# Performance work log

Hardware: AMD Instinct MI355X
Metric: run time of the kernel (lower is better)

Reference implementation:

```python
import jax, jax.numpy as jnp
import numpy as np

NUM_HEADS = 8
KERNEL = 3


def _arsinh_norm(x, w, b):
    # ArsinhNorm with scale=1.0: weight * asinh(x) + bias
    return w * jnp.arcsinh(x) + b


def _nbr_idx(L, k):
    # NATTEN neighborhood: window start clamped so the k-window stays in-bounds
    start = jnp.clip(jnp.arange(L) - k // 2, 0, L - k)
    return start[:, None] + jnp.arange(k)  # [L, k]


def _na2d(x, qkv_w, qkv_b, proj_w, proj_b, num_heads=NUM_HEADS, k=KERNEL):
    B, H, W, C = x.shape
    hd = C // num_heads
    qkv = x @ qkv_w + qkv_b                      # [B,H,W,3C]
    q, kk, v = jnp.split(qkv, 3, axis=-1)
    q = q.reshape(B, H, W, num_heads, hd) * (hd ** -0.5)
    kk = kk.reshape(B, H, W, num_heads, hd)
    v = v.reshape(B, H, W, num_heads, hd)
    ri = _nbr_idx(H, k)[:, None, :, None]        # [H,1,k,1]
    ci = _nbr_idx(W, k)[None, :, None, :]        # [1,W,1,k]
    nb_k = kk[:, ri, ci].reshape(B, H, W, k * k, num_heads, hd)  # gather 3x3 neighborhood
    nb_v = v[:, ri, ci].reshape(B, H, W, k * k, num_heads, hd)
    scores = jnp.einsum('bijnd,bijmnd->bijnm', q, nb_k)          # [B,H,W,nh,k*k]
    attn = jax.nn.softmax(scores, axis=-1)
    out = jnp.einsum('bijnm,bijmnd->bijnd', attn, nb_v).reshape(B, H, W, C)
    return out @ proj_w + proj_b


def setup_inputs() -> dict:
    key = jax.random.key(0)
    ks = jax.random.split(key, 8)
    B, H, W, C = 16, 64, 64, 256
    s = 0.02
    return {
        'h': jax.random.normal(ks[0], (B, H, W, C), dtype=jnp.float32),
        'qkv_w': jax.random.normal(ks[1], (C, 3 * C), dtype=jnp.float32) * s,
        'qkv_b': jnp.zeros((3 * C,), jnp.float32),
        'proj_w': jax.random.normal(ks[2], (C, C), dtype=jnp.float32) * s,
        'proj_b': jnp.zeros((C,), jnp.float32),
        'n1_w': jnp.ones((C,), jnp.float32),
        'n1_b': jnp.zeros((C,), jnp.float32),
        'n2_w': jnp.ones((C,), jnp.float32),
        'n2_b': jnp.zeros((C,), jnp.float32),
        'mlp_w1': jax.random.normal(ks[3], (C, 2 * C), dtype=jnp.float32) * s,
        'mlp_b1': jnp.zeros((2 * C,), jnp.float32),
        'mlp_w2': jax.random.normal(ks[4], (2 * C, C), dtype=jnp.float32) * s,
        'mlp_b2': jnp.zeros((C,), jnp.float32),
    }


def reference(h, qkv_w, qkv_b, proj_w, proj_b, n1_w, n1_b, n2_w, n2_b,
              mlp_w1, mlp_b1, mlp_w2, mlp_b2):
    h1 = _arsinh_norm(h, n1_w, n1_b)
    h = h + _na2d(h1, qkv_w, qkv_b, proj_w, proj_b)
    h2 = _arsinh_norm(h, n2_w, n2_b)
    ff = jax.nn.gelu(h2 @ mlp_w1 + mlp_b1, approximate=False) @ mlp_w2 + mlp_b2
    return h + ff
```

## Files before the change

### kernel.cpp

```cpp
#include <hip/hip_runtime.h>
#include <math.h>

typedef unsigned short u16;
typedef unsigned int u32;
typedef __attribute__((ext_vector_type(8))) short short8;
typedef __attribute__((ext_vector_type(4))) float f32x4;

__device__ __forceinline__ float b2f(u16 u) {
    return __uint_as_float(((u32)u) << 16);
}
__device__ __forceinline__ u16 f2b(float f) {
    u32 x = __float_as_uint(f);
    return (u16)((x + 0x7fffu + ((x >> 16) & 1u)) >> 16);
}
__device__ __forceinline__ float ldext(const void* p, size_t i, int isbf) {
    return isbf ? b2f(((const u16*)p)[i]) : ((const float*)p)[i];
}
__device__ __forceinline__ void stext(void* p, size_t i, int isbf, float v) {
    if (isbf) ((u16*)p)[i] = f2b(v);
    else ((float*)p)[i] = v;
}
__device__ __forceinline__ float fast_asinh(float x) {
    float ax = fabsf(x);
    float s = sqrtf(fmaf(ax, ax, 1.f));
    float l = __logf(ax + s);
    return copysignf(l, x);
}
__device__ __forceinline__ float fast_gelu(float x) {
    float x2 = x * x;
    float inner = fmaf(0.044715f * x2, x, x);
    float t = __expf(1.5957691216057308f * inner);
    return x * t * __builtin_amdgcn_rcpf(t + 1.f);
}
__device__ __forceinline__ void gl2lds16(const u16* g, u16* l) {
    __builtin_amdgcn_global_load_lds(
        (const __attribute__((address_space(1))) u32*)(const void*)g,
        (__attribute__((address_space(3))) u32*)(void*)l, 16, 0, 0);
}
__device__ __forceinline__ void unpack8(uint4 w, float* f) {
    const u32* pw = (const u32*)&w;
#pragma unroll
    for (int k = 0; k < 4; ++k) {
        f[2 * k]     = __uint_as_float(pw[k] << 16);
        f[2 * k + 1] = __uint_as_float(pw[k] & 0xffff0000u);
    }
}

__global__ void detect_k(const void* __restrict__ h, int* __restrict__ flag) {
    __shared__ int cnt;
    if (threadIdx.x == 0) cnt = 0;
    __syncthreads();
    const u16* p = (const u16*)h;
    int local = 0;
    for (int i = threadIdx.x; i < 4096; i += 256) {
        int e = (p[i] >> 7) & 0xFF;
        if (e != 0 && (e < 110 || e > 133)) local++;
    }
    atomicAdd(&cnt, local);
    __syncthreads();
    if (threadIdx.x == 0) *flag = (cnt < 256) ? 1 : 0;
}

__global__ void transpose_k(const void* __restrict__ src, u16* __restrict__ dst,
                            int R, int C, const int* __restrict__ flag) {
    int isbf = *flag;
    int idx = blockIdx.x * 256 + threadIdx.x;
    if (idx >= R * C) return;
    int r = idx / C, c = idx - r * C;
    dst[c * R + r] = f2b(ldext(src, idx, isbf));
}

__global__ void norm_k(const void* __restrict__ xb, size_t xoff,
                       const void* __restrict__ w, const void* __restrict__ b,
                       u16* __restrict__ y, const int* __restrict__ flag, int force_bf) {
    int isbf = *flag;
    int xisbf = force_bf ? 1 : isbf;
    size_t base = ((size_t)blockIdx.x * 256 + threadIdx.x) * 4;
    int c0 = (int)(base & 255);
    float v[4];
    if (xisbf) {
        uint2 raw = *reinterpret_cast<const uint2*>((const u16*)xb + xoff + base);
        const u16* px = reinterpret_cast<const u16*>(&raw);
#pragma unroll
        for (int j = 0; j < 4; ++j) v[j] = b2f(px[j]);
    } else {
        float4 r = *reinterpret_cast<const float4*>((const float*)xb + xoff + base);
        v[0] = r.x; v[1] = r.y; v[2] = r.z; v[3] = r.w;
    }
    u16 o[4];
#pragma unroll
    for (int j = 0; j < 4; ++j)
        o[j] = f2b(ldext(w, c0 + j, isbf) * fast_asinh(v[j]) + ldext(b, c0 + j, isbf));
    *reinterpret_cast<uint2*>(y + base) = *reinterpret_cast<uint2*>(o);
}

template <int EPI>
__global__ __launch_bounds__(256) void gemm_bt(
    const u16* __restrict__ A, const u16* __restrict__ BT, const void* __restrict__ bias,
    const void* __restrict__ resb, size_t resoff, void* __restrict__ outb, size_t outoff,
    int N, int K, const int* __restrict__ flag,
    const void* __restrict__ n2w, const void* __restrict__ n2b, u16* __restrict__ out2) {
    __shared__ __align__(16) u16 lA[2][128 * 32];
    __shared__ __align__(16) u16 lB[2][128 * 32];
    const int isbf = *flag;
    const int tid = threadIdx.x;
    const int lane = tid & 63;
    const int wave = tid >> 6;
    const int waveM = wave >> 1, waveN = wave & 1;

    const int gx = gridDim.x;
    int nblk = gx * gridDim.y;
    int bflat = blockIdx.y * gx + blockIdx.x;
    int L = bflat;
    if ((nblk & 7) == 0) {
        int per = nblk >> 3;
        L = (bflat & 7) * per + (bflat >> 3);
    }
    const int m0 = (L / gx) * 128;
    const int n0 = (L % gx) * 128;

    f32x4 acc[4][4];
#pragma unroll
    for (int mi = 0; mi < 4; ++mi)
#pragma unroll
        for (int ni = 0; ni < 4; ++ni)
#pragma unroll
            for (int r = 0; r < 4; ++r) acc[mi][ni][r] = 0.f;

    const int lrow = lane & 15;
    const int ko = (lane >> 4) * 8;
    const int s0 = wave * 2, s1 = wave * 2 + 1;
    const int e0a = (s0 * 64 + lane) * 8, e1a = (s1 * 64 + lane) * 8;
    const int row0 = e0a >> 5, col0 = e0a & 31;
    const int row1 = e1a >> 5, col1 = e1a & 31;

    const int NT = K >> 5;
    gl2lds16(&A[(size_t)(m0 + row0) * K + col0], &lA[0][s0 * 512]);
    gl2lds16(&BT[(size_t)(n0 + row0) * K + col0], &lB[0][s0 * 512]);
    gl2lds16(&A[(size_t)(m0 + row1) * K + col1], &lA[0][s1 * 512]);
    gl2lds16(&BT[(size_t)(n0 + row1) * K + col1], &lB[0][s1 * 512]);
    __syncthreads();

    int cur = 0;
    for (int t = 0; t < NT; ++t) {
        if (t + 1 < NT) {
            int k0 = (t + 1) << 5;
            gl2lds16(&A[(size_t)(m0 + row0) * K + k0 + col0], &lA[cur ^ 1][s0 * 512]);
            gl2lds16(&BT[(size_t)(n0 + row0) * K + k0 + col0], &lB[cur ^ 1][s0 * 512]);
            gl2lds16(&A[(size_t)(m0 + row1) * K + k0 + col1], &lA[cur ^ 1][s1 * 512]);
            gl2lds16(&BT[(size_t)(n0 + row1) * K + k0 + col1], &lB[cur ^ 1][s1 * 512]);
        }
        short8 af[4], bfr[4];
#pragma unroll
        for (int mi = 0; mi < 4; ++mi)
            af[mi] = *reinterpret_cast<const short8*>(&lA[cur][(waveM * 64 + mi * 16 + lrow) * 32 + ko]);
#pragma unroll
        for (int ni = 0; ni < 4; ++ni)
            bfr[ni] = *reinterpret_cast<const short8*>(&lB[cur][(waveN * 64 + ni * 16 + lrow) * 32 + ko]);
#pragma unroll
        for (int mi = 0; mi < 4; ++mi)
#pragma unroll
            for (int ni = 0; ni < 4; ++ni)
                acc[mi][ni] = __builtin_amdgcn_mfma_f32_16x16x32_bf16(af[mi], bfr[ni], acc[mi][ni], 0, 0, 0);
        __syncthreads();
        cur ^= 1;
    }

    const int rquad = (lane >> 4) * 4;
    const int ccol = lane & 15;
#pragma unroll
    for (int mi = 0; mi < 4; ++mi)
#pragma unroll
        for (int ni = 0; ni < 4; ++ni) {
            int colg = n0 + waveN * 64 + ni * 16 + ccol;
            float bb = ldext(bias, colg, isbf);
#pragma unroll
            for (int r = 0; r < 4; ++r) {
                int rowg = m0 + waveM * 64 + mi * 16 + rquad + r;
                size_t idx = (size_t)rowg * N + colg;
                float v = acc[mi][ni][r] + bb;
                if (EPI == 0) {
                    ((u16*)outb)[outoff + idx] = f2b(v);
                } else if (EPI == 1) {
                    ((u16*)outb)[outoff + idx] = f2b(fast_gelu(v));
                } else if (EPI == 2) {
                    v += ldext(resb, resoff + idx, isbf);
                    stext(outb, outoff + idx, isbf, v);
                } else if (EPI == 3) {
                    v += ldext(resb, resoff + idx, isbf);
                    ((u16*)outb)[outoff + idx] = f2b(v);
                } else if (EPI == 4) {
                    v += b2f(((const u16*)resb)[resoff + idx]);
                    stext(outb, outoff + idx, isbf, v);
                } else {
                    v += ldext(resb, resoff + idx, isbf);
                    ((u16*)outb)[outoff + idx] = f2b(v);
                    float y = ldext(n2w, colg, isbf) * fast_asinh(v) + ldext(n2b, colg, isbf);
                    out2[idx] = f2b(y);
                }
            }
        }
}

__global__ __launch_bounds__(256) void attn_k(const u16* __restrict__ qkv, u16* __restrict__ out) {
    const int t = blockIdx.x * 256 + threadIdx.x;
    const int head = t & 7;
    const int p = t >> 3;
    const int b = p >> 12;
    const int ij = p & 4095;
    const int i = ij >> 6, j = ij & 63;
    int r0 = i - 1; r0 = r0 < 0 ? 0 : (r0 > 61 ? 61 : r0);
    int c0 = j - 1; c0 = c0 < 0 ? 0 : (c0 > 61 ? 61 : c0);

    const u16* qp = qkv + (size_t)p * 768 + head * 32;
    float q[32];
#pragma unroll
    for (int ch = 0; ch < 4; ++ch)
        unpack8(*reinterpret_cast<const uint4*>(qp + ch * 8), q + ch * 8);

    const float qscale = 0.17677669529663687f;
    int nbp[9];
    float sc[9];
#pragma unroll
    for (int dr = 0; dr < 3; ++dr)
#pragma unroll
        for (int dc = 0; dc < 3; ++dc) {
            int nb = dr * 3 + dc;
            int np_ = b * 4096 + (r0 + dr) * 64 + (c0 + dc);
            nbp[nb] = np_;
            const u16* kp = qkv + (size_t)np_ * 768 + 256 + head * 32;
            float dot = 0.f;
#pragma unroll
            for (int ch = 0; ch < 4; ++ch) {
                float kf[8];
                unpack8(*reinterpret_cast<const uint4*>(kp + ch * 8), kf);
#pragma unroll
                for (int e = 0; e < 8; ++e) dot += q[ch * 8 + e] * kf[e];
            }
            sc[nb] = dot * qscale;
        }

    float mx = sc[0];
#pragma unroll
    for (int nb = 1; nb < 9; ++nb) mx = fmaxf(mx, sc[nb]);
    float s = 0.f;
#pragma unroll
    for (int nb = 0; nb < 9; ++nb) { sc[nb] = __expf(sc[nb] - mx); s += sc[nb]; }
    float inv = 1.f / s;

    float acc[32];
#pragma unroll
    for (int e = 0; e < 32; ++e) acc[e] = 0.f;
#pragma unroll
    for (int nb = 0; nb < 9; ++nb) {
        const u16* vp = qkv + (size_t)nbp[nb] * 768 + 512 + head * 32;
        float wgt = sc[nb] * inv;
#pragma unroll
        for (int ch = 0; ch < 4; ++ch) {
            float vf[8];
            unpack8(*reinterpret_cast<const uint4*>(vp + ch * 8), vf);
#pragma unroll
            for (int e = 0; e < 8; ++e) acc[ch * 8 + e] += wgt * vf[e];
        }
    }

    u16 ob[32];
#pragma unroll
    for (int e = 0; e < 32; ++e) ob[e] = f2b(acc[e]);
    uint4* ov = reinterpret_cast<uint4*>(ob);
    uint4* og = reinterpret_cast<uint4*>(out + (size_t)p * 256 + head * 32);
#pragma unroll
    for (int ch = 0; ch < 4; ++ch) og[ch] = ov[ch];
}

extern "C" void kernel_launch(void* const* d_in, const int* in_sizes, int n_in,
                              void* d_out, int out_size, void* d_ws, size_t ws_size,
                              hipStream_t stream) {
    const void* h      = d_in[0];
    const void* qkv_w  = d_in[1];
    const void* qkv_b  = d_in[2];
    const void* proj_w = d_in[3];
    const void* proj_b = d_in[4];
    const void* n1_w   = d_in[5];
    const void* n1_b   = d_in[6];
    const void* n2_w   = d_in[7];
    const void* n2_b   = d_in[8];
    const void* w1     = d_in[9];
    const void* b1     = d_in[10];
    const void* w2     = d_in[11];
    const void* b2     = d_in[12];

    char* ws = (char*)d_ws;
    u16* WqkvT  = (u16*)(ws + 0);
    u16* WprojT = (u16*)(ws + 393216);
    u16* W1T    = (u16*)(ws + 524288);
    u16* W2T    = (u16*)(ws + 786432);
    int* Flag   = (int*)(ws + 1048576);
    char* bufs  = ws + 1049600;

    size_t avail = ws_size > 1049600 ? ws_size - 1049600 : 0;
    int CHUNK = 4096;
    if (avail >= (size_t)65536 * 2048) CHUNK = 65536;
    else if (avail >= (size_t)16384 * 2048) CHUNK = 16384;
    else if (avail >= (size_t)8192 * 2048) CHUNK = 8192;

    u16* H1 = (u16*)bufs;
    u16* S  = (u16*)(bufs + (size_t)CHUNK * 512);

    detect_k<<<1, 256, 0, stream>>>(h, Flag);
    transpose_k<<<768, 256, 0, stream>>>(qkv_w, WqkvT, 256, 768, Flag);
    transpose_k<<<256, 256, 0, stream>>>(proj_w, WprojT, 256, 256, Flag);
    transpose_k<<<512, 256, 0, stream>>>(w1, W1T, 256, 512, Flag);
    transpose_k<<<512, 256, 0, stream>>>(w2, W2T, 512, 256, Flag);

    if (CHUNK == 65536) {
        u16* HNS = S;
        u16* T   = S + (size_t)65536 * 256;
        u16* N2  = (u16*)d_out;
        norm_k<<<16384, 256, 0, stream>>>(h, 0, n1_w, n1_b, H1, Flag, 0);
        { dim3 g(6, 512); gemm_bt<0><<<g, 256, 0, stream>>>(H1, WqkvT, qkv_b, nullptr, 0, S, 0,
                                                            768, 256, Flag, nullptr, nullptr, nullptr); }
        attn_k<<<2048, 256, 0, stream>>>(S, H1);
        { dim3 g(2, 512); gemm_bt<5><<<g, 256, 0, stream>>>(H1, WprojT, proj_b, h, 0, HNS, 0,
                                                            256, 256, Flag, n2_w, n2_b, N2); }
        { dim3 g(4, 512); gemm_bt<1><<<g, 256, 0, stream>>>(N2, W1T, b1, nullptr, 0, T, 0,
                                                            512, 256, Flag, nullptr, nullptr, nullptr); }
        { dim3 g(2, 512); gemm_bt<4><<<g, 256, 0, stream>>>(T, W2T, b2, HNS, 0, d_out, 0,
                                                            256, 512, Flag, nullptr, nullptr, nullptr); }
    } else {
        const int NCH = 65536 / CHUNK;
        for (int c = 0; c < NCH; ++c) {
            size_t off = (size_t)c * CHUNK * 256;
            norm_k<<<CHUNK / 4, 256, 0, stream>>>(h, off, n1_w, n1_b, H1, Flag, 0);
            { dim3 g(6, CHUNK / 128);
              gemm_bt<0><<<g, 256, 0, stream>>>(H1, WqkvT, qkv_b, nullptr, 0, S, 0,
                                                768, 256, Flag, nullptr, nullptr, nullptr); }
            attn_k<<<CHUNK / 32, 256, 0, stream>>>(S, H1);
            { dim3 g(2, CHUNK / 128);
              gemm_bt<2><<<g, 256, 0, stream>>>(H1, WprojT, proj_b, h, off, d_out, off,
                                                256, 256, Flag, nullptr, nullptr, nullptr); }
        }
        for (int c = 0; c < NCH; ++c) {
            size_t off = (size_t)c * CHUNK * 256;
            norm_k<<<CHUNK / 4, 256, 0, stream>>>(d_out, off, n2_w, n2_b, H1, Flag, 0);
            { dim3 g(4, CHUNK / 128);
              gemm_bt<1><<<g, 256, 0, stream>>>(H1, W1T, b1, nullptr, 0, S, 0,
                                                512, 256, Flag, nullptr, nullptr, nullptr); }
            { dim3 g(2, CHUNK / 128);
              gemm_bt<2><<<g, 256, 0, stream>>>(S, W2T, b2, d_out, off, d_out, off,
                                                256, 512, Flag, nullptr, nullptr, nullptr); }
        }
    }
}
```

Baseline: 448.5 us.

## Triple-buffer GEMM LDS tiles with vmcnt waits and a single barrier per step

Changes the GEMM main loop from double to triple buffering in LDS. It prefetches two K-tiles ahead and uses explicit s_waitcnt vmcnt plus one barrier per iteration instead of a trailing __syncthreads. K becomes a template parameter so the loop can be fully unrolled with constant addressing. This is meant to hide global-to-LDS latency and cut synchronization overhead, but it raises LDS use from 32KB to 48KB per block, which may reduce occupancy. The vmcnt counting has to match the number of outstanding loads exactly.

```diff
diff --git a/kernel.cpp b/kernel.cpp
--- a/kernel.cpp
+++ b/kernel.cpp
@@ -94,14 +94,14 @@
     *reinterpret_cast<uint2*>(y + base) = *reinterpret_cast<uint2*>(o);
 }
 
-template <int EPI>
+template <int EPI, int K>
 __global__ __launch_bounds__(256) void gemm_bt(
     const u16* __restrict__ A, const u16* __restrict__ BT, const void* __restrict__ bias,
     const void* __restrict__ resb, size_t resoff, void* __restrict__ outb, size_t outoff,
-    int N, int K, const int* __restrict__ flag,
+    int N, const int* __restrict__ flag,
     const void* __restrict__ n2w, const void* __restrict__ n2b, u16* __restrict__ out2) {
-    __shared__ __align__(16) u16 lA[2][128 * 32];
-    __shared__ __align__(16) u16 lB[2][128 * 32];
+    __shared__ __align__(16) u16 lA[3][128 * 32];
+    __shared__ __align__(16) u16 lB[3][128 * 32];
     const int isbf = *flag;
     const int tid = threadIdx.x;
     const int lane = tid & 63;
@@ -134,36 +134,43 @@
     const int row0 = e0a >> 5, col0 = e0a & 31;
     const int row1 = e1a >> 5, col1 = e1a & 31;
 
-    const int NT = K >> 5;
-    gl2lds16(&A[(size_t)(m0 + row0) * K + col0], &lA[0][s0 * 512]);
-    gl2lds16(&BT[(size_t)(n0 + row0) * K + col0], &lB[0][s0 * 512]);
-    gl2lds16(&A[(size_t)(m0 + row1) * K + col1], &lA[0][s1 * 512]);
-    gl2lds16(&BT[(size_t)(n0 + row1) * K + col1], &lB[0][s1 * 512]);
-    __syncthreads();
-
-    int cur = 0;
+    constexpr int NT = K >> 5;
+    auto STAGE = [&](int kt, int bsel) {
+        int k0 = kt << 5;
+        gl2lds16(&A[(size_t)(m0 + row0) * K + k0 + col0], &lA[bsel][s0 * 512]);
+        gl2lds16(&BT[(size_t)(n0 + row0) * K + k0 + col0], &lB[bsel][s0 * 512]);
+        gl2lds16(&A[(size_t)(m0 + row1) * K + k0 + col1], &lA[bsel][s1 * 512]);
+        gl2lds16(&BT[(size_t)(n0 + row1) * K + k0 + col1], &lB[bsel][s1 * 512]);
+    };
+
+    STAGE(0, 0);
+    STAGE(1, 1);
+
+#pragma unroll
     for (int t = 0; t < NT; ++t) {
         if (t + 1 < NT) {
-            int k0 = (t + 1) << 5;
-            gl2lds16(&A[(size_t)(m0 + row0) * K + k0 + col0], &lA[cur ^ 1][s0 * 512]);
-            gl2lds16(&BT[(size_t)(n0 + row0) * K + k0 + col0], &lB[cur ^ 1][s0 * 512]);
-            gl2lds16(&A[(size_t)(m0 + row1) * K + k0 + col1], &lA[cur ^ 1][s1 * 512]);
-            gl2lds16(&BT[(size_t)(n0 + row1) * K + k0 + col1], &lB[cur ^ 1][s1 * 512]);
-        }
+            asm volatile("s_waitcnt vmcnt(4)" ::: "memory");
+        } else {
+            asm volatile("s_waitcnt vmcnt(0)" ::: "memory");
+        }
+        __builtin_amdgcn_s_barrier();
+        __builtin_amdgcn_sched_barrier(0);
+        if (t + 2 < NT) STAGE(t + 2, (t + 2) % 3);
+
+        const u16* la = lA[t % 3];
+        const u16* lb = lB[t % 3];
         short8 af[4], bfr[4];
 #pragma unroll
         for (int mi = 0; mi < 4; ++mi)
-            af[mi] = *reinterpret_cast<const short8*>(&lA[cur][(waveM * 64 + mi * 16 + lrow) * 32 + ko]);
+            af[mi] = *reinterpret_cast<const short8*>(&la[(waveM * 64 + mi * 16 + lrow) * 32 + ko]);
 #pragma unroll
         for (int ni = 0; ni < 4; ++ni)
-            bfr[ni] = *reinterpret_cast<const short8*>(&lB[cur][(waveN * 64 + ni * 16 + lrow) * 32 + ko]);
+            bfr[ni] = *reinterpret_cast<const short8*>(&lb[(waveN * 64 + ni * 16 + lrow) * 32 + ko]);
 #pragma unroll
         for (int mi = 0; mi < 4; ++mi)
 #pragma unroll
             for (int ni = 0; ni < 4; ++ni)
                 acc[mi][ni] = __builtin_amdgcn_mfma_f32_16x16x32_bf16(af[mi], bfr[ni], acc[mi][ni], 0, 0, 0);
-        __syncthreads();
-        cur ^= 1;
     }
 
     const int rquad = (lane >> 4) * 4;
@@ -318,37 +325,37 @@
         u16* T   = S + (size_t)65536 * 256;
         u16* N2  = (u16*)d_out;
         norm_k<<<16384, 256, 0, stream>>>(h, 0, n1_w, n1_b, H1, Flag, 0);
-        { dim3 g(6, 512); gemm_bt<0><<<g, 256, 0, stream>>>(H1, WqkvT, qkv_b, nullptr, 0, S, 0,
-                                                            768, 256, Flag, nullptr, nullptr, nullptr); }
+        { dim3 g(6, 512); gemm_bt<0, 256><<<g, 256, 0, stream>>>(H1, WqkvT, qkv_b, nullptr, 0, S, 0,
+                                                                 768, Flag, nullptr, nullptr, nullptr); }
         attn_k<<<2048, 256, 0, stream>>>(S, H1);
-        { dim3 g(2, 512); gemm_bt<5><<<g, 256, 0, stream>>>(H1, WprojT, proj_b, h, 0, HNS, 0,
-                                                            256, 256, Flag, n2_w, n2_b, N2); }
-        { dim3 g(4, 512); gemm_bt<1><<<g, 256, 0, stream>>>(N2, W1T, b1, nullptr, 0, T, 0,
-                                                            512, 256, Flag, nullptr, nullptr, nullptr); }
-        { dim3 g(2, 512); gemm_bt<4><<<g, 256, 0, stream>>>(T, W2T, b2, HNS, 0, d_out, 0,
-                                                            256, 512, Flag, nullptr, nullptr, nullptr); }
+        { dim3 g(2, 512); gemm_bt<5, 256><<<g, 256, 0, stream>>>(H1, WprojT, proj_b, h, 0, HNS, 0,
+                                                                 256, Flag, n2_w, n2_b, N2); }
+        { dim3 g(4, 512); gemm_bt<1, 256><<<g, 256, 0, stream>>>(N2, W1T, b1, nullptr, 0, T, 0,
+                                                                 512, Flag, nullptr, nullptr, nullptr); }
+        { dim3 g(2, 512); gemm_bt<4, 512><<<g, 256, 0, stream>>>(T, W2T, b2, HNS, 0, d_out, 0,
+                                                                 256, Flag, nullptr, nullptr, nullptr); }
     } else {
         const int NCH = 65536 / CHUNK;
         for (int c = 0; c < NCH; ++c) {
             size_t off = (size_t)c * CHUNK * 256;
             norm_k<<<CHUNK / 4, 256, 0, stream>>>(h, off, n1_w, n1_b, H1, Flag, 0);
             { dim3 g(6, CHUNK / 128);
-              gemm_bt<0><<<g, 256, 0, stream>>>(H1, WqkvT, qkv_b, nullptr, 0, S, 0,
-                                                768, 256, Flag, nullptr, nullptr, nullptr); }
+              gemm_bt<0, 256><<<g, 256, 0, stream>>>(H1, WqkvT, qkv_b, nullptr, 0, S, 0,
+                                                     768, Flag, nullptr, nullptr, nullptr); }
             attn_k<<<CHUNK / 32, 256, 0, stream>>>(S, H1);
             { dim3 g(2, CHUNK / 128);
-              gemm_bt<2><<<g, 256, 0, stream>>>(H1, WprojT, proj_b, h, off, d_out, off,
-                                                256, 256, Flag, nullptr, nullptr, nullptr); }
+              gemm_bt<2, 256><<<g, 256, 0, stream>>>(H1, WprojT, proj_b, h, off, d_out, off,
+                                                     256, Flag, nullptr, nullptr, nullptr); }
         }
         for (int c = 0; c < NCH; ++c) {
             size_t off = (size_t)c * CHUNK * 256;
             norm_k<<<CHUNK / 4, 256, 0, stream>>>(d_out, off, n2_w, n2_b, H1, Flag, 0);
             { dim3 g(4, CHUNK / 128);
-              gemm_bt<1><<<g, 256, 0, stream>>>(H1, W1T, b1, nullptr, 0, S, 0,
-                                                512, 256, Flag, nullptr, nullptr, nullptr); }
+              gemm_bt<1, 256><<<g, 256, 0, stream>>>(H1, W1T, b1, nullptr, 0, S, 0,
+                                                     512, Flag, nullptr, nullptr, nullptr); }
             { dim3 g(2, CHUNK / 128);
-              gemm_bt<2><<<g, 256, 0, stream>>>(S, W2T, b2, d_out, off, d_out, off,
-                                                256, 512, Flag, nullptr, nullptr, nullptr); }
-        }
-    }
-}
+              gemm_bt<2, 512><<<g, 256, 0, stream>>>(S, W2T, b2, d_out, off, d_out, off,
+                                                     256, Flag, nullptr, nullptr, nullptr); }
+        }
+    }
+}
```

Result: no change. 456.2 us (+1.7%).
